# Kernel optimization log

Hardware: AMD Instinct MI355X
Metric: run time of the kernel (lower is better)

Reference implementation:

```python
import jax, jax.numpy as jnp
import numpy as np

N_NODES = 50000
N_EDGES = 800000
D_IN, D_HID, D_OUT = 128, 256, 128


def setup_inputs() -> dict:
    key = jax.random.key(0)
    ks = jax.random.split(key, 8)
    x = jax.random.normal(ks[0], (N_NODES, D_IN), dtype=jnp.float32)
    edge_src = jax.random.randint(ks[1], (N_EDGES,), 0, N_NODES, dtype=jnp.int32)
    edge_dst = jnp.sort(jax.random.randint(ks[2], (N_EDGES,), 0, N_NODES, dtype=jnp.int32))
    edge_val = jax.random.uniform(ks[3], (N_EDGES,), dtype=jnp.float32)
    eps = jnp.zeros((1,), dtype=jnp.float32)
    w1 = jax.random.normal(ks[4], (D_IN, D_HID), dtype=jnp.float32) * (1.0 / np.sqrt(D_IN))
    b1 = jnp.zeros((D_HID,), dtype=jnp.float32)
    w2 = jax.random.normal(ks[5], (D_HID, D_OUT), dtype=jnp.float32) * (1.0 / np.sqrt(D_HID))
    b2 = jnp.zeros((D_OUT,), dtype=jnp.float32)
    return {"x": x, "edge_src": edge_src, "edge_dst": edge_dst, "edge_val": edge_val,
            "eps": eps, "w1": w1, "b1": b1, "w2": w2, "b2": b2}


def reference(x, edge_src, edge_dst, edge_val, eps, w1, b1, w2, b2):
    # Sparse adjacency aggregation: (A @ x)[i] = sum_{e: dst=i} val_e * x[src_e]
    msgs = edge_val[:, None] * x[edge_src]            # [E, D_IN]
    agg = jax.ops.segment_sum(msgs, edge_dst, num_segments=N_NODES)  # [N, D_IN]
    h = agg + (1.0 + eps[0]) * x                      # AX + (1+eps)X
    # 2-layer MLP
    h = jax.nn.relu(h @ w1 + b1)                      # [N, D_HID]
    out = h @ w2 + b2                                 # [N, D_OUT]
    return out
```

## Files before the change

kernel.cpp:

```cpp
#include <hip/hip_runtime.h>
#include <hip/hip_bf16.h>
#include <cstdint>
#include <type_traits>

#define N_NODES 50000
#define N_EDGES 800000
#define D_IN 128
#define D_HID 256
#define D_OUT 128

typedef __bf16 bf16;
typedef __bf16 bf16x8 __attribute__((ext_vector_type(8)));
typedef __bf16 bf16x4 __attribute__((ext_vector_type(4)));
typedef float f32x4 __attribute__((ext_vector_type(4)));

__global__ __launch_bounds__(256) void prep_kernel(
    const float* __restrict__ x, const float* __restrict__ eps,
    const float* __restrict__ w1, const float* __restrict__ w2,
    bf16* __restrict__ aggb, bf16* __restrict__ xb,
    bf16* __restrict__ w1t, bf16* __restrict__ w2t) {
  const int i = blockIdx.x * 256 + threadIdx.x;
  const float scale = 1.0f + eps[0];
  float4 v = ((const float4*)x)[i];
  ((bf16x4*)xb)[i] = bf16x4{(bf16)v.x, (bf16)v.y, (bf16)v.z, (bf16)v.w};
  ((bf16x4*)aggb)[i] = bf16x4{(bf16)(v.x * scale), (bf16)(v.y * scale),
                              (bf16)(v.z * scale), (bf16)(v.w * scale)};
  if (i < D_IN * D_HID) {
    int k = i >> 8, n = i & 255;
    w1t[n * D_IN + k] = (bf16)w1[i];
  } else if (i < 2 * D_IN * D_HID) {
    int j = i - D_IN * D_HID;
    int k = j >> 7, n = j & 127;
    w2t[n * D_HID + k] = (bf16)w2[j];
  }
}

__device__ __forceinline__ void flush_pk(bf16* __restrict__ agg, int node,
                                         int lane, float2 acc) {
  union { struct { bf16 x, y; } h; int i; } u;
  u.h.x = (bf16)acc.x; u.h.y = (bf16)acc.y;
  const bf16* p = &agg[(long)node * D_IN + lane * 2];
  asm volatile("global_atomic_pk_add_bf16 %0, %1, off"
               :: "v"(p), "v"(u.i) : "memory");
}

__global__ __launch_bounds__(256) void edge_agg_kernel(
    const bf16* __restrict__ xb, const int* __restrict__ src,
    const int* __restrict__ dst, const float* __restrict__ val,
    bf16* __restrict__ agg) {
  const int wave = (blockIdx.x << 2) | (threadIdx.x >> 6);
  const int lane = threadIdx.x & 63;
  const int e0 = __builtin_amdgcn_readfirstlane(wave << 6);

  float2 acc = make_float2(0.f, 0.f);
  int cur = dst[e0];

  #pragma unroll 1
  for (int j = 0; j < 64; j += 16) {
    int s[16], d[16];
    float v[16];
    #pragma unroll
    for (int t = 0; t < 16; ++t) {
      s[t] = src[e0 + j + t];
      d[t] = dst[e0 + j + t];
      v[t] = val[e0 + j + t];
    }
    int g[16];
    #pragma unroll
    for (int t = 0; t < 16; ++t)
      g[t] = *(const int*)&xb[(long)s[t] * D_IN + lane * 2];
    #pragma unroll
    for (int t = 0; t < 16; ++t) {
      if (d[t] != cur) {
        flush_pk(agg, cur, lane, acc);
        acc.x = 0.f; acc.y = 0.f;
        cur = d[t];
      }
      float gx = __uint_as_float((unsigned)g[t] << 16);
      float gy = __uint_as_float((unsigned)g[t] & 0xffff0000u);
      acc.x = fmaf(v[t], gx, acc.x);
      acc.y = fmaf(v[t], gy, acc.y);
    }
  }
  flush_pk(agg, cur, lane, acc);
}

template <int KDIM, int NOUT, bool RELU, typename TC>
__global__ __launch_bounds__(256) void gemm(
    const bf16* __restrict__ A, const bf16* __restrict__ Wt,
    const float* __restrict__ bias, TC* __restrict__ C) {
  constexpr int LDL = 136;
  __shared__ alignas(16) bf16 As[64][LDL];
  __shared__ alignas(16) bf16 Bs[64][LDL];

  const int tid = threadIdx.x;
  const int m0 = blockIdx.x * 64;
  const int n0 = blockIdx.y * 64;
  const int wave = tid >> 6;
  const int lane = tid & 63;
  const int wm = (wave >> 1) * 32;
  const int wn = (wave & 1) * 32;
  const int l15 = lane & 15;
  const int quad = lane >> 4;

  f32x4 acc[2][2] = {};

  for (int kt = 0; kt < KDIM; kt += 128) {
    #pragma unroll
    for (int it = 0; it < 4; ++it) {
      int idx = tid + it * 256;
      int r = idx >> 4;
      int c8 = (idx & 15) << 3;
      int row = m0 + r; if (row >= N_NODES) row = N_NODES - 1;
      *(bf16x8*)&As[r][c8] = *(const bf16x8*)&A[(long)row * KDIM + kt + c8];
    }
    #pragma unroll
    for (int it = 0; it < 4; ++it) {
      int idx = tid + it * 256;
      int r = idx >> 4;
      int c8 = (idx & 15) << 3;
      *(bf16x8*)&Bs[r][c8] = *(const bf16x8*)&Wt[(long)(n0 + r) * KDIM + kt + c8];
    }
    __syncthreads();

    #pragma unroll
    for (int ks = 0; ks < 4; ++ks) {
      int kq = ks * 32 + quad * 8;
      bf16x8 a0 = *(const bf16x8*)&As[wm + l15][kq];
      bf16x8 a1 = *(const bf16x8*)&As[wm + 16 + l15][kq];
      bf16x8 b0 = *(const bf16x8*)&Bs[wn + l15][kq];
      bf16x8 b1 = *(const bf16x8*)&Bs[wn + 16 + l15][kq];
      acc[0][0] = __builtin_amdgcn_mfma_f32_16x16x32_bf16(a0, b0, acc[0][0], 0, 0, 0);
      acc[0][1] = __builtin_amdgcn_mfma_f32_16x16x32_bf16(a0, b1, acc[0][1], 0, 0, 0);
      acc[1][0] = __builtin_amdgcn_mfma_f32_16x16x32_bf16(a1, b0, acc[1][0], 0, 0, 0);
      acc[1][1] = __builtin_amdgcn_mfma_f32_16x16x32_bf16(a1, b1, acc[1][1], 0, 0, 0);
    }
    __syncthreads();
  }

  #pragma unroll
  for (int mf = 0; mf < 2; ++mf) {
    #pragma unroll
    for (int nf = 0; nf < 2; ++nf) {
      int col = n0 + wn + nf * 16 + l15;
      float bv = bias[col];
      #pragma unroll
      for (int r = 0; r < 4; ++r) {
        int row = m0 + wm + mf * 16 + quad * 4 + r;
        if (row < N_NODES) {
          float vv = acc[mf][nf][r] + bv;
          if constexpr (RELU) vv = fmaxf(vv, 0.f);
          if constexpr (std::is_same_v<TC, float>)
            C[(long)row * NOUT + col] = vv;
          else
            C[(long)row * NOUT + col] = (bf16)vv;
        }
      }
    }
  }
}

extern "C" void kernel_launch(void* const* d_in, const int* in_sizes, int n_in,
                              void* d_out, int out_size, void* d_ws, size_t ws_size,
                              hipStream_t stream) {
  const float* x    = (const float*)d_in[0];
  const int*   esrc = (const int*)d_in[1];
  const int*   edst = (const int*)d_in[2];
  const float* evl  = (const float*)d_in[3];
  const float* eps  = (const float*)d_in[4];
  const float* w1   = (const float*)d_in[5];
  const float* b1   = (const float*)d_in[6];
  const float* w2   = (const float*)d_in[7];
  const float* b2   = (const float*)d_in[8];
  float* out = (float*)d_out;

  bf16* aggb = (bf16*)d_ws;
  bf16* xb   = aggb + (size_t)N_NODES * D_IN;
  bf16* h    = xb + (size_t)N_NODES * D_IN;
  bf16* w1t  = h + (size_t)N_NODES * D_HID;
  bf16* w2t  = w1t + D_IN * D_HID;

  prep_kernel<<<(N_NODES * D_IN / 4) / 256, 256, 0, stream>>>(
      x, eps, w1, w2, aggb, xb, w1t, w2t);
  edge_agg_kernel<<<N_EDGES / 256, 256, 0, stream>>>(xb, esrc, edst, evl, aggb);
  gemm<D_IN, D_HID, true, bf16>
      <<<dim3((N_NODES + 63) / 64, D_HID / 64), 256, 0, stream>>>(aggb, w1t, b1, h);
  gemm<D_HID, D_OUT, false, float>
      <<<dim3((N_NODES + 63) / 64, D_OUT / 64), 256, 0, stream>>>(h, w2t, b2, out);
}
```

Measured before the change: 157.2 us.

## Fuse prep, edge aggregation and both GEMMs into one cooperative persistent kernel

```diff
diff --git a/kernel.cpp b/kernel.cpp
--- a/kernel.cpp
+++ b/kernel.cpp
@@ -1,7 +1,10 @@
 #include <hip/hip_runtime.h>
 #include <hip/hip_bf16.h>
+#include <hip/hip_cooperative_groups.h>
 #include <cstdint>
 #include <type_traits>
+
+namespace cg = cooperative_groups;
 
 #define N_NODES 50000
 #define N_EDGES 800000
@@ -9,10 +12,211 @@
 #define D_HID 256
 #define D_OUT 128
 
+#define MT1 782
+#define EDGE_CHUNKS 12500
+
 typedef __bf16 bf16;
 typedef __bf16 bf16x8 __attribute__((ext_vector_type(8)));
 typedef __bf16 bf16x4 __attribute__((ext_vector_type(4)));
 typedef float f32x4 __attribute__((ext_vector_type(4)));
+
+__device__ __forceinline__ void flush_pk(bf16* __restrict__ agg, int node,
+                                         int lane, float2 acc) {
+  union { struct { bf16 x, y; } h; int i; } u;
+  u.h.x = (bf16)acc.x; u.h.y = (bf16)acc.y;
+  const bf16* p = &agg[(long)node * D_IN + lane * 2];
+  asm volatile("global_atomic_pk_add_bf16 %0, %1, off"
+               :: "v"(p), "v"(u.i) : "memory");
+}
+
+__global__ __launch_bounds__(256) void mega_kernel(
+    const float* __restrict__ x, const float* __restrict__ eps,
+    const float* __restrict__ w1, const float* __restrict__ w2,
+    const float* __restrict__ b1, const float* __restrict__ b2,
+    const int* __restrict__ esrc, const int* __restrict__ edst,
+    const float* __restrict__ evl,
+    bf16* __restrict__ aggb, bf16* __restrict__ xb,
+    bf16* __restrict__ w1t, bf16* __restrict__ w2t,
+    bf16* __restrict__ h, float* __restrict__ out) {
+  __shared__ alignas(16) bf16 smem[192 * 136];
+  cg::grid_group grid = cg::this_grid();
+
+  const int tid = threadIdx.x;
+  const int gtid = blockIdx.x * 256 + tid;
+  const int nthr = gridDim.x * 256;
+  const int wave = tid >> 6;
+  const int lane = tid & 63;
+  const int l15 = lane & 15;
+  const int quad = lane >> 4;
+
+  {
+    const float scale = 1.0f + eps[0];
+    for (int i = gtid; i < N_NODES * D_IN / 4; i += nthr) {
+      float4 v = ((const float4*)x)[i];
+      ((bf16x4*)xb)[i] = bf16x4{(bf16)v.x, (bf16)v.y, (bf16)v.z, (bf16)v.w};
+      ((bf16x4*)aggb)[i] = bf16x4{(bf16)(v.x * scale), (bf16)(v.y * scale),
+                                  (bf16)(v.z * scale), (bf16)(v.w * scale)};
+    }
+    for (int i = gtid; i < D_IN * D_HID; i += nthr) {
+      int k = i >> 8, n = i & 255;
+      w1t[n * D_IN + k] = (bf16)w1[i];
+    }
+    for (int i = gtid; i < D_HID * D_OUT; i += nthr) {
+      int k = i >> 7, n = i & 127;
+      w2t[n * D_HID + k] = (bf16)w2[i];
+    }
+  }
+  grid.sync();
+
+  {
+    const int waveId = (blockIdx.x << 2) | wave;
+    const int totWaves = gridDim.x << 2;
+    for (int c = waveId; c < EDGE_CHUNKS; c += totWaves) {
+      const int e0 = __builtin_amdgcn_readfirstlane(c << 6);
+      float2 acc = make_float2(0.f, 0.f);
+      int cur = edst[e0];
+      #pragma unroll 1
+      for (int j = 0; j < 64; j += 16) {
+        int s[16], d[16];
+        float v[16];
+        #pragma unroll
+        for (int t = 0; t < 16; ++t) {
+          s[t] = esrc[e0 + j + t];
+          d[t] = edst[e0 + j + t];
+          v[t] = evl[e0 + j + t];
+        }
+        int g[16];
+        #pragma unroll
+        for (int t = 0; t < 16; ++t)
+          g[t] = *(const int*)&xb[(long)s[t] * D_IN + lane * 2];
+        #pragma unroll
+        for (int t = 0; t < 16; ++t) {
+          if (d[t] != cur) {
+            flush_pk(aggb, cur, lane, acc);
+            acc.x = 0.f; acc.y = 0.f;
+            cur = d[t];
+          }
+          float gx = __uint_as_float((unsigned)g[t] << 16);
+          float gy = __uint_as_float((unsigned)g[t] & 0xffff0000u);
+          acc.x = fmaf(v[t], gx, acc.x);
+          acc.y = fmaf(v[t], gy, acc.y);
+        }
+      }
+      flush_pk(aggb, cur, lane, acc);
+    }
+  }
+  grid.sync();
+
+  {
+    bf16* As = smem;
+    bf16* Bs = smem + 64 * 136;
+    for (int t = blockIdx.x; t < MT1 * 2; t += gridDim.x) {
+      const int m0 = (t >> 1) * 64;
+      const int n0 = (t & 1) * 128;
+      #pragma unroll
+      for (int it = 0; it < 4; ++it) {
+        int idx = tid + it * 256;
+        int r = idx >> 4, c8 = (idx & 15) << 3;
+        int row = m0 + r; if (row >= N_NODES) row = N_NODES - 1;
+        *(bf16x8*)&As[r * 136 + c8] = *(const bf16x8*)&aggb[(long)row * D_IN + c8];
+      }
+      #pragma unroll
+      for (int it = 0; it < 8; ++it) {
+        int idx = tid + it * 256;
+        int r = idx >> 4, c8 = (idx & 15) << 3;
+        *(bf16x8*)&Bs[r * 136 + c8] = *(const bf16x8*)&w1t[(long)(n0 + r) * D_IN + c8];
+      }
+      __syncthreads();
+      const int wm = (wave & 1) * 32;
+      const int wn = (wave >> 1) * 64;
+      f32x4 acc[2][4] = {};
+      #pragma unroll
+      for (int ks = 0; ks < 4; ++ks) {
+        int kq = ks * 32 + quad * 8;
+        bf16x8 a0 = *(const bf16x8*)&As[(wm + l15) * 136 + kq];
+        bf16x8 a1 = *(const bf16x8*)&As[(wm + 16 + l15) * 136 + kq];
+        bf16x8 bf[4];
+        #pragma unroll
+        for (int nf = 0; nf < 4; ++nf)
+          bf[nf] = *(const bf16x8*)&Bs[(wn + nf * 16 + l15) * 136 + kq];
+        #pragma unroll
+        for (int nf = 0; nf < 4; ++nf) {
+          acc[0][nf] = __builtin_amdgcn_mfma_f32_16x16x32_bf16(a0, bf[nf], acc[0][nf], 0, 0, 0);
+          acc[1][nf] = __builtin_amdgcn_mfma_f32_16x16x32_bf16(a1, bf[nf], acc[1][nf], 0, 0, 0);
+        }
+      }
+      __syncthreads();
+      #pragma unroll
+      for (int nf = 0; nf < 4; ++nf) {
+        int col = n0 + wn + nf * 16 + l15;
+        float bv = b1[col];
+        #pragma unroll
+        for (int mf = 0; mf < 2; ++mf)
+          #pragma unroll
+          for (int r = 0; r < 4; ++r) {
+            int row = m0 + wm + mf * 16 + quad * 4 + r;
+            if (row < N_NODES)
+              h[(long)row * D_HID + col] = (bf16)fmaxf(acc[mf][nf][r] + bv, 0.f);
+          }
+      }
+    }
+  }
+  grid.sync();
+
+  {
+    bf16* As = smem;
+    bf16* Bs = smem + 64 * 136;
+    for (int t = blockIdx.x; t < MT1 * 2; t += gridDim.x) {
+      const int m0 = (t >> 1) * 64;
+      const int n0 = (t & 1) * 64;
+      const int wm = (wave >> 1) * 32;
+      const int wn = (wave & 1) * 32;
+      f32x4 acc[2][2] = {};
+      for (int kt = 0; kt < D_HID; kt += 128) {
+        #pragma unroll
+        for (int it = 0; it < 4; ++it) {
+          int idx = tid + it * 256;
+          int r = idx >> 4, c8 = (idx & 15) << 3;
+          int row = m0 + r; if (row >= N_NODES) row = N_NODES - 1;
+          *(bf16x8*)&As[r * 136 + c8] = *(const bf16x8*)&h[(long)row * D_HID + kt + c8];
+        }
+        #pragma unroll
+        for (int it = 0; it < 4; ++it) {
+          int idx = tid + it * 256;
+          int r = idx >> 4, c8 = (idx & 15) << 3;
+          *(bf16x8*)&Bs[r * 136 + c8] = *(const bf16x8*)&w2t[(long)(n0 + r) * D_HID + kt + c8];
+        }
+        __syncthreads();
+        #pragma unroll
+        for (int ks = 0; ks < 4; ++ks) {
+          int kq = ks * 32 + quad * 8;
+          bf16x8 a0 = *(const bf16x8*)&As[(wm + l15) * 136 + kq];
+          bf16x8 a1 = *(const bf16x8*)&As[(wm + 16 + l15) * 136 + kq];
+          bf16x8 b0 = *(const bf16x8*)&Bs[(wn + l15) * 136 + kq];
+          bf16x8 b1f = *(const bf16x8*)&Bs[(wn + 16 + l15) * 136 + kq];
+          acc[0][0] = __builtin_amdgcn_mfma_f32_16x16x32_bf16(a0, b0, acc[0][0], 0, 0, 0);
+          acc[0][1] = __builtin_amdgcn_mfma_f32_16x16x32_bf16(a0, b1f, acc[0][1], 0, 0, 0);
+          acc[1][0] = __builtin_amdgcn_mfma_f32_16x16x32_bf16(a1, b0, acc[1][0], 0, 0, 0);
+          acc[1][1] = __builtin_amdgcn_mfma_f32_16x16x32_bf16(a1, b1f, acc[1][1], 0, 0, 0);
+        }
+        __syncthreads();
+      }
+      #pragma unroll
+      for (int nf = 0; nf < 2; ++nf) {
+        int col = n0 + wn + nf * 16 + l15;
+        float bv = b2[col];
+        #pragma unroll
+        for (int mf = 0; mf < 2; ++mf)
+          #pragma unroll
+          for (int r = 0; r < 4; ++r) {
+            int row = m0 + wm + mf * 16 + quad * 4 + r;
+            if (row < N_NODES)
+              out[(long)row * D_OUT + col] = acc[mf][nf][r] + bv;
+          }
+      }
+    }
+  }
+}
 
 __global__ __launch_bounds__(256) void prep_kernel(
     const float* __restrict__ x, const float* __restrict__ eps,
@@ -35,15 +239,6 @@
   }
 }
 
-__device__ __forceinline__ void flush_pk(bf16* __restrict__ agg, int node,
-                                         int lane, float2 acc) {
-  union { struct { bf16 x, y; } h; int i; } u;
-  u.h.x = (bf16)acc.x; u.h.y = (bf16)acc.y;
-  const bf16* p = &agg[(long)node * D_IN + lane * 2];
-  asm volatile("global_atomic_pk_add_bf16 %0, %1, off"
-               :: "v"(p), "v"(u.i) : "memory");
-}
-
 __global__ __launch_bounds__(256) void edge_agg_kernel(
     const bf16* __restrict__ xb, const int* __restrict__ src,
     const int* __restrict__ dst, const float* __restrict__ val,
@@ -51,19 +246,15 @@
   const int wave = (blockIdx.x << 2) | (threadIdx.x >> 6);
   const int lane = threadIdx.x & 63;
   const int e0 = __builtin_amdgcn_readfirstlane(wave << 6);
-
   float2 acc = make_float2(0.f, 0.f);
   int cur = dst[e0];
-
   #pragma unroll 1
   for (int j = 0; j < 64; j += 16) {
     int s[16], d[16];
     float v[16];
     #pragma unroll
     for (int t = 0; t < 16; ++t) {
-      s[t] = src[e0 + j + t];
-      d[t] = dst[e0 + j + t];
-      v[t] = val[e0 + j + t];
+      s[t] = src[e0 + j + t]; d[t] = dst[e0 + j + t]; v[t] = val[e0 + j + t];
     }
     int g[16];
     #pragma unroll
@@ -92,7 +283,6 @@
   constexpr int LDL = 136;
   __shared__ alignas(16) bf16 As[64][LDL];
   __shared__ alignas(16) bf16 Bs[64][LDL];
-
   const int tid = threadIdx.x;
   const int m0 = blockIdx.x * 64;
   const int n0 = blockIdx.y * 64;
@@ -102,27 +292,22 @@
   const int wn = (wave & 1) * 32;
   const int l15 = lane & 15;
   const int quad = lane >> 4;
-
   f32x4 acc[2][2] = {};
-
   for (int kt = 0; kt < KDIM; kt += 128) {
     #pragma unroll
     for (int it = 0; it < 4; ++it) {
       int idx = tid + it * 256;
-      int r = idx >> 4;
-      int c8 = (idx & 15) << 3;
+      int r = idx >> 4, c8 = (idx & 15) << 3;
       int row = m0 + r; if (row >= N_NODES) row = N_NODES - 1;
       *(bf16x8*)&As[r][c8] = *(const bf16x8*)&A[(long)row * KDIM + kt + c8];
     }
     #pragma unroll
     for (int it = 0; it < 4; ++it) {
       int idx = tid + it * 256;
-      int r = idx >> 4;
-      int c8 = (idx & 15) << 3;
+      int r = idx >> 4, c8 = (idx & 15) << 3;
       *(bf16x8*)&Bs[r][c8] = *(const bf16x8*)&Wt[(long)(n0 + r) * KDIM + kt + c8];
     }
     __syncthreads();
-
     #pragma unroll
     for (int ks = 0; ks < 4; ++ks) {
       int kq = ks * 32 + quad * 8;
@@ -137,9 +322,8 @@
     }
     __syncthreads();
   }
-
   #pragma unroll
-  for (int mf = 0; mf < 2; ++mf) {
+  for (int mf = 0; mf < 2; ++mf)
     #pragma unroll
     for (int nf = 0; nf < 2; ++nf) {
       int col = n0 + wn + nf * 16 + l15;
@@ -157,7 +341,6 @@
         }
       }
     }
-  }
 }
 
 extern "C" void kernel_launch(void* const* d_in, const int* in_sizes, int n_in,
@@ -180,11 +363,27 @@
   bf16* w1t  = h + (size_t)N_NODES * D_HID;
   bf16* w2t  = w1t + D_IN * D_HID;
 
-  prep_kernel<<<(N_NODES * D_IN / 4) / 256, 256, 0, stream>>>(
-      x, eps, w1, w2, aggb, xb, w1t, w2t);
-  edge_agg_kernel<<<N_EDGES / 256, 256, 0, stream>>>(xb, esrc, edst, evl, aggb);
-  gemm<D_IN, D_HID, true, bf16>
-      <<<dim3((N_NODES + 63) / 64, D_HID / 64), 256, 0, stream>>>(aggb, w1t, b1, h);
-  gemm<D_HID, D_OUT, false, float>
-      <<<dim3((N_NODES + 63) / 64, D_OUT / 64), 256, 0, stream>>>(h, w2t, b2, out);
-}
+  int perCU = 0;
+  hipError_t qerr = hipOccupancyMaxActiveBlocksPerMultiprocessor(
+      &perCU, (const void*)mega_kernel, 256, 0);
+  if (qerr != hipSuccess || perCU < 1) perCU = 1;
+  int nblk = perCU * 256;
+  if (nblk > MT1 * 2) nblk = MT1 * 2;
+
+  void* args[] = {(void*)&x, (void*)&eps, (void*)&w1, (void*)&w2,
+                  (void*)&b1, (void*)&b2, (void*)&esrc, (void*)&edst,
+                  (void*)&evl, (void*)&aggb, (void*)&xb, (void*)&w1t,
+                  (void*)&w2t, (void*)&h, (void*)&out};
+  hipError_t err = hipLaunchCooperativeKernel(
+      (const void*)mega_kernel, dim3(nblk), dim3(256), args, 0, stream);
+
+  if (err != hipSuccess) {
+    prep_kernel<<<(N_NODES * D_IN / 4) / 256, 256, 0, stream>>>(
+        x, eps, w1, w2, aggb, xb, w1t, w2t);
+    edge_agg_kernel<<<N_EDGES / 256, 256, 0, stream>>>(xb, esrc, edst, evl, aggb);
+    gemm<D_IN, D_HID, true, bf16>
+        <<<dim3((N_NODES + 63) / 64, D_HID / 64), 256, 0, stream>>>(aggb, w1t, b1, h);
+    gemm<D_HID, D_OUT, false, float>
+        <<<dim3((N_NODES + 63) / 64, D_OUT / 64), 256, 0, stream>>>(h, w2t, b2, out);
+  }
+}
```

Measured after the change: 390.1 us. 148% more time.

## Replace atomic edge aggregation with node-partitioned CSR-style ownership and fused self term

Applied to the files above, without the earlier changes.

```diff
diff --git a/kernel.cpp b/kernel.cpp
--- a/kernel.cpp
+++ b/kernel.cpp
@@ -8,6 +8,7 @@
 #define D_IN 128
 #define D_HID 256
 #define D_OUT 128
+#define NODES_PER_WAVE 16
 
 typedef __bf16 bf16;
 typedef __bf16 bf16x8 __attribute__((ext_vector_type(8)));
@@ -15,16 +16,12 @@
 typedef float f32x4 __attribute__((ext_vector_type(4)));
 
 __global__ __launch_bounds__(256) void prep_kernel(
-    const float* __restrict__ x, const float* __restrict__ eps,
-    const float* __restrict__ w1, const float* __restrict__ w2,
-    bf16* __restrict__ aggb, bf16* __restrict__ xb,
+    const float* __restrict__ x, const float* __restrict__ w1,
+    const float* __restrict__ w2, bf16* __restrict__ xb,
     bf16* __restrict__ w1t, bf16* __restrict__ w2t) {
   const int i = blockIdx.x * 256 + threadIdx.x;
-  const float scale = 1.0f + eps[0];
   float4 v = ((const float4*)x)[i];
   ((bf16x4*)xb)[i] = bf16x4{(bf16)v.x, (bf16)v.y, (bf16)v.z, (bf16)v.w};
-  ((bf16x4*)aggb)[i] = bf16x4{(bf16)(v.x * scale), (bf16)(v.y * scale),
-                              (bf16)(v.z * scale), (bf16)(v.w * scale)};
   if (i < D_IN * D_HID) {
     int k = i >> 8, n = i & 255;
     w1t[n * D_IN + k] = (bf16)w1[i];
@@ -35,35 +32,55 @@
   }
 }
 
-__device__ __forceinline__ void flush_pk(bf16* __restrict__ agg, int node,
-                                         int lane, float2 acc) {
+__device__ __forceinline__ void store_row(bf16* __restrict__ agg, int node,
+                                          int lane, float2 a) {
   union { struct { bf16 x, y; } h; int i; } u;
-  u.h.x = (bf16)acc.x; u.h.y = (bf16)acc.y;
-  const bf16* p = &agg[(long)node * D_IN + lane * 2];
-  asm volatile("global_atomic_pk_add_bf16 %0, %1, off"
-               :: "v"(p), "v"(u.i) : "memory");
-}
-
-__global__ __launch_bounds__(256) void edge_agg_kernel(
-    const bf16* __restrict__ xb, const int* __restrict__ src,
-    const int* __restrict__ dst, const float* __restrict__ val,
+  u.h.x = (bf16)a.x; u.h.y = (bf16)a.y;
+  *(int*)&agg[(long)node * D_IN + lane * 2] = u.i;
+}
+
+__global__ __launch_bounds__(256) void edge_csr_kernel(
+    const float* __restrict__ x, const bf16* __restrict__ xb,
+    const int* __restrict__ esrc, const int* __restrict__ edst,
+    const float* __restrict__ evl, const float* __restrict__ eps,
     bf16* __restrict__ agg) {
-  const int wave = (blockIdx.x << 2) | (threadIdx.x >> 6);
+  const int w = (blockIdx.x << 2) | (threadIdx.x >> 6);
   const int lane = threadIdx.x & 63;
-  const int e0 = __builtin_amdgcn_readfirstlane(wave << 6);
-
-  float2 acc = make_float2(0.f, 0.f);
-  int cur = dst[e0];
+  const int n_begin = w * NODES_PER_WAVE;
+  if (n_begin >= N_NODES) return;
+  const int n_end = n_begin + NODES_PER_WAVE;
+  const float scale = 1.0f + eps[0];
+  const float2* x2 = (const float2*)x;
+
+  float2 self[NODES_PER_WAVE];
+  #pragma unroll
+  for (int n = 0; n < NODES_PER_WAVE; ++n) {
+    float2 q = x2[(long)(n_begin + n) * 64 + lane];
+    self[n] = make_float2(scale * q.x, scale * q.y);
+  }
+
+  int lo = 0, hi = N_EDGES;
+  while (lo < hi) {
+    int mid = (lo + hi) >> 1;
+    if (edst[mid] < n_begin) lo = mid + 1; else hi = mid;
+  }
+  int e = __builtin_amdgcn_readfirstlane(lo);
+
+  int cur = n_begin;
+  float2 acc = self[0];
+  bool done = false;
 
   #pragma unroll 1
-  for (int j = 0; j < 64; j += 16) {
+  while (!done) {
     int s[16], d[16];
     float v[16];
     #pragma unroll
     for (int t = 0; t < 16; ++t) {
-      s[t] = src[e0 + j + t];
-      d[t] = dst[e0 + j + t];
-      v[t] = val[e0 + j + t];
+      int et = e + t;
+      bool ok = et < N_EDGES;
+      s[t] = ok ? esrc[et] : 0;
+      d[t] = ok ? edst[et] : N_NODES;
+      v[t] = ok ? evl[et] : 0.f;
     }
     int g[16];
     #pragma unroll
@@ -71,18 +88,31 @@
       g[t] = *(const int*)&xb[(long)s[t] * D_IN + lane * 2];
     #pragma unroll
     for (int t = 0; t < 16; ++t) {
-      if (d[t] != cur) {
-        flush_pk(agg, cur, lane, acc);
-        acc.x = 0.f; acc.y = 0.f;
-        cur = d[t];
+      if (!done) {
+        if (d[t] != cur) {
+          if (d[t] >= n_end) {
+            done = true;
+          } else {
+            store_row(agg, cur, lane, acc);
+            for (int n = cur + 1; n < d[t]; ++n)
+              store_row(agg, n, lane, self[n - n_begin]);
+            cur = d[t];
+            acc = self[cur - n_begin];
+          }
+        }
+        if (!done) {
+          float gx = __uint_as_float((unsigned)g[t] << 16);
+          float gy = __uint_as_float((unsigned)g[t] & 0xffff0000u);
+          acc.x = fmaf(v[t], gx, acc.x);
+          acc.y = fmaf(v[t], gy, acc.y);
+        }
       }
-      float gx = __uint_as_float((unsigned)g[t] << 16);
-      float gy = __uint_as_float((unsigned)g[t] & 0xffff0000u);
-      acc.x = fmaf(v[t], gx, acc.x);
-      acc.y = fmaf(v[t], gy, acc.y);
-    }
-  }
-  flush_pk(agg, cur, lane, acc);
+    }
+    e += 16;
+  }
+  store_row(agg, cur, lane, acc);
+  for (int n = cur + 1; n < n_end; ++n)
+    store_row(agg, n, lane, self[n - n_begin]);
 }
 
 template <int KDIM, int NOUT, bool RELU, typename TC>
@@ -92,7 +122,6 @@
   constexpr int LDL = 136;
   __shared__ alignas(16) bf16 As[64][LDL];
   __shared__ alignas(16) bf16 Bs[64][LDL];
-
   const int tid = threadIdx.x;
   const int m0 = blockIdx.x * 64;
   const int n0 = blockIdx.y * 64;
@@ -102,27 +131,22 @@
   const int wn = (wave & 1) * 32;
   const int l15 = lane & 15;
   const int quad = lane >> 4;
-
   f32x4 acc[2][2] = {};
-
   for (int kt = 0; kt < KDIM; kt += 128) {
     #pragma unroll
     for (int it = 0; it < 4; ++it) {
       int idx = tid + it * 256;
-      int r = idx >> 4;
-      int c8 = (idx & 15) << 3;
+      int r = idx >> 4, c8 = (idx & 15) << 3;
       int row = m0 + r; if (row >= N_NODES) row = N_NODES - 1;
       *(bf16x8*)&As[r][c8] = *(const bf16x8*)&A[(long)row * KDIM + kt + c8];
     }
     #pragma unroll
     for (int it = 0; it < 4; ++it) {
       int idx = tid + it * 256;
-      int r = idx >> 4;
-      int c8 = (idx & 15) << 3;
+      int r = idx >> 4, c8 = (idx & 15) << 3;
       *(bf16x8*)&Bs[r][c8] = *(const bf16x8*)&Wt[(long)(n0 + r) * KDIM + kt + c8];
     }
     __syncthreads();
-
     #pragma unroll
     for (int ks = 0; ks < 4; ++ks) {
       int kq = ks * 32 + quad * 8;
@@ -137,9 +161,8 @@
     }
     __syncthreads();
   }
-
   #pragma unroll
-  for (int mf = 0; mf < 2; ++mf) {
+  for (int mf = 0; mf < 2; ++mf)
     #pragma unroll
     for (int nf = 0; nf < 2; ++nf) {
       int col = n0 + wn + nf * 16 + l15;
@@ -157,7 +180,6 @@
         }
       }
     }
-  }
 }
 
 extern "C" void kernel_launch(void* const* d_in, const int* in_sizes, int n_in,
@@ -174,17 +196,18 @@
   const float* b2   = (const float*)d_in[8];
   float* out = (float*)d_out;
 
-  bf16* aggb = (bf16*)d_ws;
-  bf16* xb   = aggb + (size_t)N_NODES * D_IN;
-  bf16* h    = xb + (size_t)N_NODES * D_IN;
-  bf16* w1t  = h + (size_t)N_NODES * D_HID;
-  bf16* w2t  = w1t + D_IN * D_HID;
+  bf16* agg = (bf16*)d_ws;
+  bf16* xb  = agg + (size_t)N_NODES * D_IN;
+  bf16* h   = xb + (size_t)N_NODES * D_IN;
+  bf16* w1t = h + (size_t)N_NODES * D_HID;
+  bf16* w2t = w1t + D_IN * D_HID;
 
   prep_kernel<<<(N_NODES * D_IN / 4) / 256, 256, 0, stream>>>(
-      x, eps, w1, w2, aggb, xb, w1t, w2t);
-  edge_agg_kernel<<<N_EDGES / 256, 256, 0, stream>>>(xb, esrc, edst, evl, aggb);
+      x, w1, w2, xb, w1t, w2t);
+  edge_csr_kernel<<<(N_NODES / NODES_PER_WAVE + 3) / 4, 256, 0, stream>>>(
+      x, xb, esrc, edst, evl, eps, agg);
   gemm<D_IN, D_HID, true, bf16>
-      <<<dim3((N_NODES + 63) / 64, D_HID / 64), 256, 0, stream>>>(aggb, w1t, b1, h);
+      <<<dim3((N_NODES + 63) / 64, D_HID / 64), 256, 0, stream>>>(agg, w1t, b1, h);
   gemm<D_HID, D_OUT, false, float>
       <<<dim3((N_NODES + 63) / 64, D_OUT / 64), 256, 0, stream>>>(h, w2t, b2, out);
 }
```

Result: slower. 247.7 us (+57.6%).
